# Kernel optimization log

Measured on AMD Instinct MI355X. Metric: run time of the kernel, lower is better.

The kernel has to match this reference:

```python
import jax, jax.numpy as jnp
import numpy as np

OUT_CHN, IN_CHN, K = 256, 256, 3
STRIDE, PAD = 1, 1


def setup_inputs() -> dict:
    key = jax.random.key(0)
    kx, kw, ks = jax.random.split(key, 3)
    x = jax.random.normal(kx, (32, IN_CHN, 56, 56), dtype=jnp.float32)
    # flat (out*in*k*k, 1) parameter, small positive init as in the torch module
    weights = jax.random.uniform(kw, (OUT_CHN * IN_CHN * K * K, 1), dtype=jnp.float32) * 0.001
    # real_scaling_factor: mean of a small random (1,out,k,k) tensor over dims 3,2,0 -> (1,out,1,1)
    sf = jax.random.uniform(ks, (1, OUT_CHN, K, K), dtype=jnp.float32) * 0.001
    real_scaling_factor = jnp.mean(jnp.abs(sf), axis=(0, 2, 3), keepdims=True)
    return {"x": x, "weights": weights, "real_scaling_factor": real_scaling_factor}


def reference(x, weights, real_scaling_factor):
    real_w = weights.reshape(OUT_CHN, IN_CHN, K, K)
    # STE binarization: forward value = sign(w), gradient of clamp(w,-1,1)
    clipped = jnp.clip(real_w, -1.0, 1.0)
    binary_w = jax.lax.stop_gradient(jnp.sign(real_w) - clipped) + clipped
    y = jax.lax.conv_general_dilated(
        x, binary_w,
        window_strides=(STRIDE, STRIDE),
        padding=[(PAD, PAD), (PAD, PAD)],
        dimension_numbers=("NCHW", "OIHW", "NCHW"),
    )
    # per-output-channel scale, broadcast over N,H,W
    return y * real_scaling_factor
```

## Files before the change

kernel.cpp:

```cpp
#include <hip/hip_runtime.h>
#include <hip/hip_bf16.h>
#include <stdint.h>

#define NIMG 32
#define CHN 256
#define HW 56
#define PH 58
#define XP_ELEMS ((size_t)NIMG*PH*PH*CHN)
#define WT_ELEMS ((size_t)9*CHN*CHN)
#define OUT_ELEMS ((size_t)NIMG*CHN*HW*HW)
#define NKT 36

typedef __attribute__((ext_vector_type(8))) short short8;
typedef __attribute__((ext_vector_type(4))) float floatx4;

#define GLDS(gp, lbyte) __builtin_amdgcn_global_load_lds( \
    (const __attribute__((address_space(1))) void*)(gp), \
    (__attribute__((address_space(3))) void*)((char*)L + (lbyte)), 16, 0, 0)

__device__ inline unsigned short f2bf(float f) {
    union { float f; uint32_t u; } v; v.f = f;
    uint32_t u = v.u;
    return (unsigned short)((u + 0x7FFFu + ((u >> 16) & 1u)) >> 16);
}

__global__ void wprep(const float* __restrict__ wflat, unsigned short* __restrict__ Wt) {
    int o = blockIdx.x * 256 + threadIdx.x;
    int rs = o >> 16, ko = (o >> 8) & 255, c = o & 255;
    float w = wflat[ko * 2304 + c * 9 + rs];
    Wt[o] = (w > 0.f) ? 0x3F80u : (w < 0.f ? 0xBF80u : 0u);
}

__global__ void xprep(const float* __restrict__ x, unsigned short* __restrict__ Xp) {
    __shared__ unsigned short tile[56 * 264];
    int b = blockIdx.x;
    int n = b / 56, h = b - n * 56;
    const float* xr = x + ((size_t)n * CHN) * (HW*HW) + h * HW;
    int tid = threadIdx.x;
    #pragma unroll 4
    for (int it = 0; it < 28; ++it) {
        int i = it * 256 + tid;
        int c2 = i / 56, w = i - c2 * 56, c = c2 * 2;
        float f0 = xr[(size_t)c * 3136 + w];
        float f1 = xr[(size_t)(c + 1) * 3136 + w];
        uint32_t u = (uint32_t)f2bf(f0) | ((uint32_t)f2bf(f1) << 16);
        *(uint32_t*)&tile[w * 264 + c] = u;
    }
    __syncthreads();
    unsigned short* op = Xp + (((size_t)n * PH + (h + 1)) * PH + 1) * CHN;
    #pragma unroll
    for (int it = 0; it < 7; ++it) {
        int chunk = it * 256 + tid;
        int w = chunk >> 5, c0 = (chunk & 31) * 8;
        short8 v = *(const short8*)&tile[w * 264 + c0];
        *(short8*)&op[w * 256 + c0] = v;
    }
}

__global__ void __launch_bounds__(512)
bconv8(const unsigned short* __restrict__ Xp, const unsigned short* __restrict__ Wt,
       const float* __restrict__ sf, float* __restrict__ out) {
    extern __shared__ unsigned short L[];
    const int tid  = threadIdx.x;
    const int lane = tid & 63, wv = tid >> 6;
    const int wm = wv >> 2, wn = wv & 3;
    const int bm = blockIdx.x;

    const int r0 = tid >> 3;
    const int sx = (tid & 7) ^ (r0 & 7);
    uint32_t offA[2][2], offB[2][2];
    #pragma unroll
    for (int hf = 0; hf < 2; ++hf)
        #pragma unroll
        for (int i = 0; i < 2; ++i) {
            int row = hf * 128 + i * 64 + r0;
            int p = bm * 256 + row;
            int n = p / 3136, hwp = p - n * 3136;
            int h = hwp / 56,  w = hwp - h * 56;
            offA[hf][i] = (uint32_t)(((((n * 58 + h) * 58 + w) * 256) + sx * 8) * 2);
            offB[hf][i] = (uint32_t)((row * 256 + sx * 8) * 2);
        }
    const uint32_t ldst0 = (uint32_t)wv * 1024u;

#define STAGE_A(kt, hf, b) do { \
    int _rs = (kt) >> 2; int _dr = _rs / 3, _dc = _rs - _dr * 3; \
    uint32_t _ko = (uint32_t)((_dr * 58 + _dc) * 512 + ((kt) & 3) * 128); \
    uint32_t _lb = (uint32_t)(((b) * 4 + (hf)) * 16384) + ldst0; \
    GLDS((const char*)Xp + offA[hf][0] + _ko, _lb); \
    GLDS((const char*)Xp + offA[hf][1] + _ko, _lb + 8192u); \
} while (0)

#define STAGE_B(kt, hf, b) do { \
    uint32_t _ko = (uint32_t)((kt) >> 2) * 131072u + (uint32_t)(((kt) & 3) * 128); \
    uint32_t _lb = (uint32_t)(((b) * 4 + 2 + (hf)) * 16384) + ldst0; \
    GLDS((const char*)Wt + offB[hf][0] + _ko, _lb); \
    GLDS((const char*)Wt + offB[hf][1] + _ko, _lb + 8192u); \
} while (0)

    const int rA = lane & 15, hs = lane >> 4, xm = lane & 7;
    const int sl0 = ((hs)     ^ xm) * 8;
    const int sl1 = ((4 + hs) ^ xm) * 8;

    floatx4 acc[8][4];
    #pragma unroll
    for (int mf = 0; mf < 8; ++mf)
        #pragma unroll
        for (int nf = 0; nf < 4; ++nf) acc[mf][nf] = (floatx4){0.f, 0.f, 0.f, 0.f};

    STAGE_A(0, 0, 0); STAGE_A(0, 1, 0); STAGE_B(0, 0, 0); STAGE_B(0, 1, 0);
    STAGE_A(1, 0, 1); STAGE_A(1, 1, 1);
    asm volatile("s_waitcnt vmcnt(4)" ::: "memory");
    __builtin_amdgcn_s_barrier();

    short8 a0[4][2], a1[4][2], b0[2][2], b1[2][2];

    for (int j = 0; j < NKT; ++j) {
        const int buf = j & 1, ob = buf ^ 1;
        const uint32_t sA = (uint32_t)(buf * 4 + wm) * 8192u + (uint32_t)(rA * 64);
        const uint32_t sB = (uint32_t)(buf * 4 + 2 + (wn >> 1)) * 8192u
                          + (uint32_t)((wn & 1) * 4096) + (uint32_t)(rA * 64);
        #pragma unroll
        for (int mf = 0; mf < 4; ++mf) {
            a0[mf][0] = *(const short8*)&L[sA + mf * 1024 + sl0];
            a0[mf][1] = *(const short8*)&L[sA + mf * 1024 + sl1];
        }
        #pragma unroll
        for (int nf = 0; nf < 2; ++nf) {
            b0[nf][0] = *(const short8*)&L[sB + nf * 1024 + sl0];
            b0[nf][1] = *(const short8*)&L[sB + nf * 1024 + sl1];
        }
        if (j < NKT - 1) STAGE_B(j + 1, 0, ob);
        __builtin_amdgcn_s_barrier();
        __builtin_amdgcn_s_setprio(1);
        #pragma unroll
        for (int mf = 0; mf < 4; ++mf)
            #pragma unroll
            for (int nf = 0; nf < 2; ++nf) {
                acc[mf][nf] = __builtin_amdgcn_mfma_f32_16x16x32_bf16(a0[mf][0], b0[nf][0], acc[mf][nf], 0, 0, 0);
                acc[mf][nf] = __builtin_amdgcn_mfma_f32_16x16x32_bf16(a0[mf][1], b0[nf][1], acc[mf][nf], 0, 0, 0);
            }
        __builtin_amdgcn_s_setprio(0);
        __builtin_amdgcn_s_barrier();
        #pragma unroll
        for (int mf = 0; mf < 4; ++mf) {
            a1[mf][0] = *(const short8*)&L[sA + (4 + mf) * 1024 + sl0];
            a1[mf][1] = *(const short8*)&L[sA + (4 + mf) * 1024 + sl1];
        }
        if (j < NKT - 1) STAGE_B(j + 1, 1, ob);
        __builtin_amdgcn_s_barrier();
        __builtin_amdgcn_s_setprio(1);
        #pragma unroll
        for (int mf = 0; mf < 4; ++mf)
            #pragma unroll
            for (int nf = 0; nf < 2; ++nf) {
                acc[4 + mf][nf] = __builtin_amdgcn_mfma_f32_16x16x32_bf16(a1[mf][0], b0[nf][0], acc[4 + mf][nf], 0, 0, 0);
                acc[4 + mf][nf] = __builtin_amdgcn_mfma_f32_16x16x32_bf16(a1[mf][1], b0[nf][1], acc[4 + mf][nf], 0, 0, 0);
            }
        __builtin_amdgcn_s_setprio(0);
        __builtin_amdgcn_s_barrier();
        #pragma unroll
        for (int nf = 0; nf < 2; ++nf) {
            b1[nf][0] = *(const short8*)&L[sB + (2 + nf) * 1024 + sl0];
            b1[nf][1] = *(const short8*)&L[sB + (2 + nf) * 1024 + sl1];
        }
        if (j < NKT - 2) STAGE_A(j + 2, 0, buf);
        __builtin_amdgcn_s_barrier();
        __builtin_amdgcn_s_setprio(1);
        #pragma unroll
        for (int mf = 0; mf < 4; ++mf)
            #pragma unroll
            for (int nf = 0; nf < 2; ++nf) {
                acc[mf][2 + nf] = __builtin_amdgcn_mfma_f32_16x16x32_bf16(a0[mf][0], b1[nf][0], acc[mf][2 + nf], 0, 0, 0);
                acc[mf][2 + nf] = __builtin_amdgcn_mfma_f32_16x16x32_bf16(a0[mf][1], b1[nf][1], acc[mf][2 + nf], 0, 0, 0);
            }
        __builtin_amdgcn_s_setprio(0);
        __builtin_amdgcn_s_barrier();
        if (j < NKT - 2) {
            STAGE_A(j + 2, 1, buf);
            asm volatile("s_waitcnt vmcnt(4)" ::: "memory");
        } else {
            asm volatile("s_waitcnt vmcnt(0)" ::: "memory");
        }
        __builtin_amdgcn_s_barrier();
        __builtin_amdgcn_s_setprio(1);
        #pragma unroll
        for (int mf = 0; mf < 4; ++mf)
            #pragma unroll
            for (int nf = 0; nf < 2; ++nf) {
                acc[4 + mf][2 + nf] = __builtin_amdgcn_mfma_f32_16x16x32_bf16(a1[mf][0], b1[nf][0], acc[4 + mf][2 + nf], 0, 0, 0);
                acc[4 + mf][2 + nf] = __builtin_amdgcn_mfma_f32_16x16x32_bf16(a1[mf][1], b1[nf][1], acc[4 + mf][2 + nf], 0, 0, 0);
            }
        __builtin_amdgcn_s_setprio(0);
        __builtin_amdgcn_s_barrier();
    }

    const int p00 = bm * 256 + wm * 128 + hs * 4;
    #pragma unroll
    for (int nf = 0; nf < 4; ++nf) {
        int ko = wn * 64 + nf * 16 + rA;
        float sc = sf[ko];
        #pragma unroll
        for (int mf = 0; mf < 8; ++mf) {
            int p = p00 + mf * 16;
            int ni = p / 3136, hwp = p - ni * 3136;
            floatx4 v = acc[mf][nf];
            floatx4 o = {v.x * sc, v.y * sc, v.z * sc, v.w * sc};
            *(floatx4*)&out[(size_t)ni * 802816 + (size_t)ko * 3136 + hwp] = o;
        }
    }
#undef STAGE_A
#undef STAGE_B
}

__global__ void naive_conv(const float* __restrict__ x, const float* __restrict__ wflat,
                           const float* __restrict__ sf, float* __restrict__ out) {
    int idx = blockIdx.x * 256 + threadIdx.x;
    int w = idx % 56, t = idx / 56;
    int h = t % 56; t /= 56;
    int ko = t % 256; int n = t / 256;
    float acc = 0.f;
    for (int c = 0; c < 256; ++c) {
        const float* xc = x + ((size_t)n * 256 + c) * 3136;
        const float* wc = wflat + ((size_t)ko * 256 + c) * 9;
        #pragma unroll
        for (int r = 0; r < 3; ++r) {
            int hh = h + r - 1;
            if (hh < 0 || hh >= 56) continue;
            #pragma unroll
            for (int s = 0; s < 3; ++s) {
                int ww = w + s - 1;
                if (ww < 0 || ww >= 56) continue;
                float wvv = wc[r * 3 + s];
                float sgn = (wvv > 0.f) ? 1.f : ((wvv < 0.f) ? -1.f : 0.f);
                acc += sgn * xc[hh * 56 + ww];
            }
        }
    }
    out[idx] = acc * sf[ko];
}

extern "C" void kernel_launch(void* const* d_in, const int* in_sizes, int n_in,
                              void* d_out, int out_size, void* d_ws, size_t ws_size,
                              hipStream_t stream) {
    const float* x     = (const float*)d_in[0];
    const float* wflat = (const float*)d_in[1];
    const float* sf    = (const float*)d_in[2];
    float* out = (float*)d_out;

    const size_t need = XP_ELEMS * 2 + WT_ELEMS * 2;
    if (ws_size < need) {
        naive_conv<<<(int)(OUT_ELEMS / 256), 256, 0, stream>>>(x, wflat, sf, out);
        return;
    }
    unsigned short* Xp = (unsigned short*)d_ws;
    unsigned short* Wt = Xp + XP_ELEMS;

    (void)hipFuncSetAttribute((const void*)bconv8,
                              hipFuncAttributeMaxDynamicSharedMemorySize, 131072);

    hipMemsetAsync(Xp, 0, XP_ELEMS * 2, stream);
    wprep<<<2304, 256, 0, stream>>>(wflat, Wt);
    xprep<<<NIMG * HW, 256, 0, stream>>>(x, Xp);
    bconv8<<<392, 512, 131072, stream>>>(Xp, Wt, sf, out);
}
```

Before: 324.0 us.

## Shrink M tile to 224 rows for better CU balance and zero only halo

Reduces the per-block output-pixel tile from 256 to 224, so the grid grows from 392 to 448 blocks and wave quantization over the CUs improves. Each wave now computes 7 M fragments instead of 8, with clamped/duplicated loads filling the unused LDS rows. The full-buffer memset of the padded input is replaced by a small kernel that zeroes only the halo border. The trade-off is slightly lower MFMA reuse per block and some redundant global loads.

```diff
diff --git a/kernel.cpp b/kernel.cpp
--- a/kernel.cpp
+++ b/kernel.cpp
@@ -10,6 +10,8 @@
 #define WT_ELEMS ((size_t)9*CHN*CHN)
 #define OUT_ELEMS ((size_t)NIMG*CHN*HW*HW)
 #define NKT 36
+#define BM 224
+#define NBLK 448
 
 typedef __attribute__((ext_vector_type(8))) short short8;
 typedef __attribute__((ext_vector_type(4))) float floatx4;
@@ -29,6 +31,19 @@
     int rs = o >> 16, ko = (o >> 8) & 255, c = o & 255;
     float w = wflat[ko * 2304 + c * 9 + rs];
     Wt[o] = (w > 0.f) ? 0x3F80u : (w < 0.f ? 0xBF80u : 0u);
+}
+
+__global__ void halo_zero(unsigned short* __restrict__ Xp) {
+    int idx = blockIdx.x * 256 + threadIdx.x;
+    int c2 = idx & 127;
+    int t  = idx >> 7;
+    int ci = t % 228, n = t / 228;
+    int h, w;
+    if (ci < 58)       { h = 0;        w = ci; }
+    else if (ci < 116) { h = 57;       w = ci - 58; }
+    else if (ci < 172) { h = ci - 115; w = 0; }
+    else               { h = ci - 171; w = 57; }
+    *(uint32_t*)&Xp[(((size_t)n * PH + h) * PH + w) * CHN + c2 * 2] = 0u;
 }
 
 __global__ void xprep(const float* __restrict__ x, unsigned short* __restrict__ Xp) {
@@ -73,37 +88,41 @@
     for (int hf = 0; hf < 2; ++hf)
         #pragma unroll
         for (int i = 0; i < 2; ++i) {
-            int row = hf * 128 + i * 64 + r0;
-            int p = bm * 256 + row;
+            int rowA = hf * 112 + i * 64 + r0;
+            if (rowA > 223) rowA = 223;
+            int p = bm * BM + rowA;
             int n = p / 3136, hwp = p - n * 3136;
             int h = hwp / 56,  w = hwp - h * 56;
             offA[hf][i] = (uint32_t)(((((n * 58 + h) * 58 + w) * 256) + sx * 8) * 2);
-            offB[hf][i] = (uint32_t)((row * 256 + sx * 8) * 2);
-        }
-    const uint32_t ldst0 = (uint32_t)wv * 1024u;
-
-#define STAGE_A(kt, hf, b) do { \
-    int _rs = (kt) >> 2; int _dr = _rs / 3, _dc = _rs - _dr * 3; \
-    uint32_t _ko = (uint32_t)((_dr * 58 + _dc) * 512 + ((kt) & 3) * 128); \
-    uint32_t _lb = (uint32_t)(((b) * 4 + (hf)) * 16384) + ldst0; \
-    GLDS((const char*)Xp + offA[hf][0] + _ko, _lb); \
-    GLDS((const char*)Xp + offA[hf][1] + _ko, _lb + 8192u); \
+            int rowB = hf * 128 + i * 64 + r0;
+            offB[hf][i] = (uint32_t)((rowB * 256 + sx * 8) * 2);
+        }
+    const uint32_t wv1k = (uint32_t)wv * 1024u;
+
+#define KOA(kt) ({ int _rs = (kt) >> 2; int _dr = _rs / 3, _dc = _rs - _dr * 3; \
+                   (uint32_t)((_dr * 58 + _dc) * 512 + ((kt) & 3) * 128); })
+#define KOB(kt) ((uint32_t)(((kt) >> 2) * 131072 + ((kt) & 3) * 128))
+
+#define STAGE_A(kt, hf, b) do { uint32_t _k = KOA(kt); \
+    uint32_t _sec = (uint32_t)(b) * 65536u + (uint32_t)(hf) * 16384u; \
+    GLDS((const char*)Xp + offA[hf][0] + _k, _sec + wv1k); \
+    if (wv < 6) GLDS((const char*)Xp + offA[hf][1] + _k, _sec + 8192u + wv1k); \
+    else        GLDS((const char*)Xp + offA[hf][0] + _k, _sec + 8192u + wv1k);  \
 } while (0)
 
-#define STAGE_B(kt, hf, b) do { \
-    uint32_t _ko = (uint32_t)((kt) >> 2) * 131072u + (uint32_t)(((kt) & 3) * 128); \
-    uint32_t _lb = (uint32_t)(((b) * 4 + 2 + (hf)) * 16384) + ldst0; \
-    GLDS((const char*)Wt + offB[hf][0] + _ko, _lb); \
-    GLDS((const char*)Wt + offB[hf][1] + _ko, _lb + 8192u); \
+#define STAGE_B(kt, hf, b) do { uint32_t _k = KOB(kt); \
+    uint32_t _sec = (uint32_t)(b) * 65536u + 32768u + (uint32_t)(hf) * 16384u; \
+    GLDS((const char*)Wt + offB[hf][0] + _k, _sec + wv1k); \
+    GLDS((const char*)Wt + offB[hf][1] + _k, _sec + 8192u + wv1k); \
 } while (0)
 
     const int rA = lane & 15, hs = lane >> 4, xm = lane & 7;
     const int sl0 = ((hs)     ^ xm) * 8;
     const int sl1 = ((4 + hs) ^ xm) * 8;
 
-    floatx4 acc[8][4];
-    #pragma unroll
-    for (int mf = 0; mf < 8; ++mf)
+    floatx4 acc[7][4];
+    #pragma unroll
+    for (int mf = 0; mf < 7; ++mf)
         #pragma unroll
         for (int nf = 0; nf < 4; ++nf) acc[mf][nf] = (floatx4){0.f, 0.f, 0.f, 0.f};
 
@@ -112,12 +131,12 @@
     asm volatile("s_waitcnt vmcnt(4)" ::: "memory");
     __builtin_amdgcn_s_barrier();
 
-    short8 a0[4][2], a1[4][2], b0[2][2], b1[2][2];
+    short8 a0[4][2], a1[3][2], b0[2][2], b1[2][2];
 
     for (int j = 0; j < NKT; ++j) {
         const int buf = j & 1, ob = buf ^ 1;
-        const uint32_t sA = (uint32_t)(buf * 4 + wm) * 8192u + (uint32_t)(rA * 64);
-        const uint32_t sB = (uint32_t)(buf * 4 + 2 + (wn >> 1)) * 8192u
+        const uint32_t sA = (uint32_t)buf * 32768u + (uint32_t)wm * 8192u + (uint32_t)(rA * 64);
+        const uint32_t sB = (uint32_t)buf * 32768u + 16384u + (uint32_t)((wn >> 1) * 8192)
                           + (uint32_t)((wn & 1) * 4096) + (uint32_t)(rA * 64);
         #pragma unroll
         for (int mf = 0; mf < 4; ++mf) {
@@ -142,7 +161,7 @@
         __builtin_amdgcn_s_setprio(0);
         __builtin_amdgcn_s_barrier();
         #pragma unroll
-        for (int mf = 0; mf < 4; ++mf) {
+        for (int mf = 0; mf < 3; ++mf) {
             a1[mf][0] = *(const short8*)&L[sA + (4 + mf) * 1024 + sl0];
             a1[mf][1] = *(const short8*)&L[sA + (4 + mf) * 1024 + sl1];
         }
@@ -150,7 +169,7 @@
         __builtin_amdgcn_s_barrier();
         __builtin_amdgcn_s_setprio(1);
         #pragma unroll
-        for (int mf = 0; mf < 4; ++mf)
+        for (int mf = 0; mf < 3; ++mf)
             #pragma unroll
             for (int nf = 0; nf < 2; ++nf) {
                 acc[4 + mf][nf] = __builtin_amdgcn_mfma_f32_16x16x32_bf16(a1[mf][0], b0[nf][0], acc[4 + mf][nf], 0, 0, 0);
@@ -184,7 +203,7 @@
         __builtin_amdgcn_s_barrier();
         __builtin_amdgcn_s_setprio(1);
         #pragma unroll
-        for (int mf = 0; mf < 4; ++mf)
+        for (int mf = 0; mf < 3; ++mf)
             #pragma unroll
             for (int nf = 0; nf < 2; ++nf) {
                 acc[4 + mf][2 + nf] = __builtin_amdgcn_mfma_f32_16x16x32_bf16(a1[mf][0], b1[nf][0], acc[4 + mf][2 + nf], 0, 0, 0);
@@ -194,13 +213,13 @@
         __builtin_amdgcn_s_barrier();
     }
 
-    const int p00 = bm * 256 + wm * 128 + hs * 4;
+    const int p00 = bm * BM + wm * 112 + hs * 4;
     #pragma unroll
     for (int nf = 0; nf < 4; ++nf) {
         int ko = wn * 64 + nf * 16 + rA;
         float sc = sf[ko];
         #pragma unroll
-        for (int mf = 0; mf < 8; ++mf) {
+        for (int mf = 0; mf < 7; ++mf) {
             int p = p00 + mf * 16;
             int ni = p / 3136, hwp = p - ni * 3136;
             floatx4 v = acc[mf][nf];
@@ -210,6 +229,8 @@
     }
 #undef STAGE_A
 #undef STAGE_B
+#undef KOA
+#undef KOB
 }
 
 __global__ void naive_conv(const float* __restrict__ x, const float* __restrict__ wflat,
@@ -258,8 +279,8 @@
     (void)hipFuncSetAttribute((const void*)bconv8,
                               hipFuncAttributeMaxDynamicSharedMemorySize, 131072);
 
-    hipMemsetAsync(Xp, 0, XP_ELEMS * 2, stream);
+    halo_zero<<<(32 * 228 * 128) / 256, 256, 0, stream>>>(Xp);
     wprep<<<2304, 256, 0, stream>>>(wflat, Wt);
     xprep<<<NIMG * HW, 256, 0, stream>>>(x, Xp);
-    bconv8<<<392, 512, 131072, stream>>>(Xp, Wt, sf, out);
-}
+    bconv8<<<NBLK, 512, 131072, stream>>>(Xp, Wt, sf, out);
+}
```

Result: no change. 322.4 us (-0.5%).
